# Kernel optimization log

Measured on AMD Instinct MI355X. Metric: run time of the kernel, lower is better.

The kernel has to match this reference:

```python
import jax, jax.numpy as jnp
import numpy as np

VOCAB = 40000
EMB = 128
INNER = 128
Q_LEN = 20


def setup_inputs() -> dict:
    key = jax.random.key(0)
    ks = jax.random.split(key, 16)
    B, S, NB = 32, 512, 20
    std = 0.1
    inp = {
        "memories": jax.random.normal(ks[0], (B, S, NB, EMB), jnp.float32),
        "stories": jax.random.normal(ks[1], (B, S, EMB), jnp.float32),
        "stories_mask": jnp.ones((B, S), jnp.float32),
        "queries": jax.random.randint(ks[2], (B, Q_LEN), 0, VOCAB, jnp.int32),
        "keys": jax.random.randint(ks[3], (NB,), 0, VOCAB, jnp.int32),
        # learned parameters
        "emb_table": jax.random.normal(ks[4], (VOCAB, EMB), jnp.float32) * std,
        "mult_mask": jnp.ones((Q_LEN, EMB), jnp.float32),
        "A": jax.random.normal(ks[5], (EMB, INNER), jnp.float32) * std,
        "Bm": jax.random.normal(ks[6], (EMB, INNER), jnp.float32) * std,
        "C": jax.random.normal(ks[7], (EMB, INNER), jnp.float32) * std,
        "v": jnp.ones((INNER,), jnp.float32),
        "D": jax.random.normal(ks[8], (EMB, INNER), jnp.float32) * std,
        "E": jax.random.normal(ks[9], (EMB, INNER), jnp.float32) * std,
        "F": jax.random.normal(ks[10], (EMB, INNER), jnp.float32) * std,
        "w": jnp.ones((INNER,), jnp.float32),
        "H": jax.random.normal(ks[11], (EMB, EMB), jnp.float32) * std,
        "R": jax.random.normal(ks[12], (EMB, VOCAB), jnp.float32) * std,
    }
    return inp


def reference(memories, stories, stories_mask, queries, keys,
              emb_table, mult_mask, A, Bm, C, v, D, E, F, w, H, R):
    # _reduce_query: embed tokens, apply positional multiplicative mask, sum over positions
    u = jnp.sum(emb_table[queries] * mult_mask, axis=1)            # [B, emb]

    # intratemporal (Bahdanau-style) attention over memory blocks
    ia = jnp.einsum('bsne,ei->bsni', memories, A)                  # [B,S,NB,inner]
    kb = emb_table[keys] @ Bm                                      # [NB,inner]
    qc = u @ C                                                     # [B,inner]
    intr_align = jnp.sum(v * jnp.tanh(ia + kb[None, None] + qc[:, None, None]), axis=3)  # [B,S,NB]
    intr_attn = jax.nn.softmax(intr_align, axis=2)[..., None]      # [B,S,NB,1]
    temporal_memory = jnp.sum(intr_attn * memories, axis=2)        # [B,S,emb]

    # temporal attention over story sentences (with sentence term E, softmax activation)
    td = temporal_memory @ D                                       # [B,S,inner]
    te = stories @ E                                               # [B,S,inner]
    tf = (u @ F)[:, None]                                          # [B,1,inner]
    temporal_align_unmasked = jnp.sum(w * jnp.tanh(td + te + tf), axis=2)  # [B,S]
    temporal_align = temporal_align_unmasked * stories_mask
    # softmax branch: additive -inf mask where stories_mask == 0 (inf*0 NaNs zeroed in torch)
    masked_logits = jnp.where(stories_mask != 0, temporal_align, -jnp.inf)
    temporal_attn = jax.nn.softmax(masked_logits, axis=1)          # [B,S]

    # output readout (standard memory-network head)
    o = jnp.sum(temporal_attn[..., None] * temporal_memory, axis=1)  # [B,emb]
    logits = (o + u @ H) @ R                                         # [B,vocab]
    return logits
```

## Files before the change

kernel.cpp:

```cpp
#include <hip/hip_runtime.h>
#include <hip/hip_bf16.h>

#define B_   32
#define S_   512
#define NB_  20
#define EMB_ 128
#define VOC_ 40000

typedef float f32x4 __attribute__((ext_vector_type(4)));
typedef __bf16 bf16x8 __attribute__((ext_vector_type(8)));

union Frag {
  uint4 u;
  bf16x8 b;
  unsigned short s[8];
};

__device__ __forceinline__ unsigned short f2bf(float x){
  unsigned u = __float_as_uint(x);
  unsigned r = (u + 0x7FFFu + ((u>>16)&1u)) >> 16;
  return (unsigned short)r;
}
__device__ __forceinline__ float bf2f(unsigned short s){
  return __uint_as_float(((unsigned)s)<<16);
}
__device__ __forceinline__ float tanh_fast(float x){
  float xx = fminf(fmaxf(x, -15.f), 15.f);
  float e = __expf(2.f*xx);
  return (e-1.f)/(e+1.f);
}

__global__ __launch_bounds__(128) void prep_kernel(
    const int* __restrict__ queries, const int* __restrict__ keys,
    const float* __restrict__ emb, const float* __restrict__ mmask,
    const float* __restrict__ A, const float* __restrict__ Bm,
    const float* __restrict__ C, const float* __restrict__ D,
    const float* __restrict__ E, const float* __restrict__ F,
    const float* __restrict__ H,
    float* __restrict__ qc_w, float* __restrict__ tf_w,
    float* __restrict__ uh_w, float* __restrict__ kb_w,
    unsigned short* __restrict__ afragH, unsigned short* __restrict__ afragL,
    unsigned short* __restrict__ w2fragH, unsigned short* __restrict__ w2fragL)
{
  int bid = blockIdx.x, tid = threadIdx.x;
  if (bid < 32) {
    __shared__ float ulds[128];
    int b = bid;
    float s = 0.f;
    for (int q=0;q<NB_;q++){
      int tok = queries[b*NB_+q];
      s += emb[tok*128+tid]*mmask[q*128+tid];
    }
    ulds[tid] = s;
    __syncthreads();
    float sq=0.f, sf=0.f, sh=0.f;
    for (int e=0;e<128;e++){
      float uv = ulds[e];
      sq += uv*C[e*128+tid];
      sf += uv*F[e*128+tid];
      sh += uv*H[e*128+tid];
    }
    qc_w[b*128+tid]=sq; tf_w[b*128+tid]=sf; uh_w[b*128+tid]=sh;
  } else if (bid < 52) {
    __shared__ float ek[128];
    int n = bid-32;
    int tok = keys[n];
    ek[tid] = emb[tok*128+tid];
    __syncthreads();
    float s=0.f;
    for (int e=0;e<128;e++) s += ek[e]*Bm[e*128+tid];
    kb_w[n*128+tid] = s;
  } else if (bid < 60) {
    int a = bid-52;
    for (int cc=0;cc<2;cc++){
      int c = (a*128+tid)*2+cc;
      int lane = c&63, kc = (c>>6)&3, nt = c>>8;
      int n2 = nt*16 + (lane&15);
      int k0 = kc*32 + (lane>>4)*8;
      alignas(16) unsigned short th[8], tl[8];
      #pragma unroll
      for (int j=0;j<8;j++){
        float x = A[(k0+j)*128+n2];
        unsigned short h = f2bf(x);
        th[j] = h;
        tl[j] = f2bf(x - bf2f(h));
      }
      *(uint4*)(afragH + c*8) = *(const uint4*)th;
      *(uint4*)(afragL + c*8) = *(const uint4*)tl;
    }
  } else {
    int wb = bid-60;
    for (int cc=0;cc<2;cc++){
      int c = (wb*128+tid)*2+cc;
      int lane = c&63, kc = (c>>6)&7, nt = c>>9;
      int n2 = nt*16 + (lane&15);
      int k0 = kc*32 + (lane>>4)*8;
      alignas(16) unsigned short th[8], tl[8];
      #pragma unroll
      for (int j=0;j<8;j++){
        int k = k0+j;
        float x = (k<128) ? D[k*128+n2] : E[(k-128)*128+n2];
        unsigned short h = f2bf(x);
        th[j] = h;
        tl[j] = f2bf(x - bf2f(h));
      }
      *(uint4*)(w2fragH + c*8) = *(const uint4*)th;
      *(uint4*)(w2fragL + c*8) = *(const uint4*)tl;
    }
  }
}

__global__ __launch_bounds__(256) void k2a_kernel(
    const float* __restrict__ mem,
    const unsigned short* __restrict__ afragH, const unsigned short* __restrict__ afragL,
    const float* __restrict__ kb_w, const float* __restrict__ qc_w,
    const float* __restrict__ vvec, float* __restrict__ tm_w)
{
  __shared__ unsigned short mfrH[5*4*64*8];
  __shared__ unsigned short mfrL[5*4*64*8];
  __shared__ float alignP[4*80];
  __shared__ float aligns[80];
  __shared__ float attns[80];

  int g = blockIdx.x, tid = threadIdx.x;
  int b = g >> 7;

  const float4* gm = (const float4*)(mem) + (size_t)g*2560;
  #pragma unroll
  for (int it=0; it<10; ++it){
    int i4 = tid + it*256;
    float4 d = gm[i4];
    int e4 = i4*4;
    int row = e4 >> 7;
    int k0 = e4 & 127;
    int mt = row >> 4;
    int lane = (((k0>>3)&3)<<4) | (row & 15);
    int chunk = (mt*4 + (k0>>5))*64 + lane;
    int sa = chunk*8 + (k0 & 7);
    unsigned short hx=f2bf(d.x), hy=f2bf(d.y), hz=f2bf(d.z), hw=f2bf(d.w);
    *(uint2*)(mfrH + sa) = make_uint2((unsigned)hx|((unsigned)hy<<16),
                                      (unsigned)hz|((unsigned)hw<<16));
    unsigned short lx=f2bf(d.x-bf2f(hx)), ly=f2bf(d.y-bf2f(hy));
    unsigned short lz=f2bf(d.z-bf2f(hz)), lw=f2bf(d.w-bf2f(hw));
    *(uint2*)(mfrL + sa) = make_uint2((unsigned)lx|((unsigned)ly<<16),
                                      (unsigned)lz|((unsigned)lw<<16));
  }
  __syncthreads();

  int w = tid>>6, lane = tid&63;
  int lo16_ = lane & 15, hi16_ = lane >> 4;
  int nt0 = 2*w, nt1 = 2*w+1;

  f32x4 acc[5][2];
  #pragma unroll
  for (int mt=0;mt<5;mt++){ acc[mt][0]=(f32x4)(0.f); acc[mt][1]=(f32x4)(0.f); }

  #pragma unroll
  for (int kc=0;kc<4;kc++){
    Frag b0h, b0l, b1h, b1l;
    b0h.u = *(const uint4*)(afragH + ((size_t)(nt0*4+kc)*64 + lane)*8);
    b0l.u = *(const uint4*)(afragL + ((size_t)(nt0*4+kc)*64 + lane)*8);
    b1h.u = *(const uint4*)(afragH + ((size_t)(nt1*4+kc)*64 + lane)*8);
    b1l.u = *(const uint4*)(afragL + ((size_t)(nt1*4+kc)*64 + lane)*8);
    #pragma unroll
    for (int mt=0;mt<5;mt++){
      Frag ah, al;
      ah.u = *(const uint4*)(mfrH + ((mt*4+kc)*64 + lane)*8);
      al.u = *(const uint4*)(mfrL + ((mt*4+kc)*64 + lane)*8);
      acc[mt][0] = __builtin_amdgcn_mfma_f32_16x16x32_bf16(ah.b, b0h.b, acc[mt][0], 0,0,0);
      acc[mt][0] = __builtin_amdgcn_mfma_f32_16x16x32_bf16(al.b, b0h.b, acc[mt][0], 0,0,0);
      acc[mt][0] = __builtin_amdgcn_mfma_f32_16x16x32_bf16(ah.b, b0l.b, acc[mt][0], 0,0,0);
      acc[mt][1] = __builtin_amdgcn_mfma_f32_16x16x32_bf16(ah.b, b1h.b, acc[mt][1], 0,0,0);
      acc[mt][1] = __builtin_amdgcn_mfma_f32_16x16x32_bf16(al.b, b1h.b, acc[mt][1], 0,0,0);
      acc[mt][1] = __builtin_amdgcn_mfma_f32_16x16x32_bf16(ah.b, b1l.b, acc[mt][1], 0,0,0);
    }
  }

  #pragma unroll
  for (int mt=0;mt<5;mt++){
    #pragma unroll
    for (int r=0;r<4;r++){
      unsigned row = mt*16 + hi16_*4 + r;
      unsigned p = row/20u;
      unsigned n = row - p*20u;
      float part = 0.f;
      #pragma unroll
      for (int t2=0;t2<2;t2++){
        int col = (2*w+t2)*16 + lo16_;
        float z = acc[mt][t2][r] + kb_w[n*128+col] + qc_w[b*128+col];
        part += vvec[col]*tanh_fast(z);
      }
      part += __shfl_xor(part, 1);
      part += __shfl_xor(part, 2);
      part += __shfl_xor(part, 4);
      part += __shfl_xor(part, 8);
      if (lo16_ == 0) alignP[w*80+row] = part;
    }
  }
  __syncthreads();
  if (tid < 80){
    aligns[tid] = alignP[tid] + alignP[80+tid] + alignP[160+tid] + alignP[240+tid];
  }
  __syncthreads();
  if (tid < 4){
    float mx = -1e30f;
    for (int n=0;n<NB_;n++) mx = fmaxf(mx, aligns[tid*NB_+n]);
    float s = 0.f;
    for (int n=0;n<NB_;n++){ float e = __expf(aligns[tid*NB_+n]-mx); attns[tid*NB_+n]=e; s+=e; }
    float inv = 1.f/s;
    for (int n=0;n<NB_;n++) attns[tid*NB_+n] *= inv;
  }
  __syncthreads();

  if (tid < 128){
    int p2 = tid>>5, e0 = (tid&31)*4;
    float4 o = make_float4(0.f,0.f,0.f,0.f);
    #pragma unroll
    for (int n=0;n<NB_;n++){
      int row = p2*NB_+n;
      float a = attns[row];
      int mt = row>>4;
      int lane2 = (((e0>>3)&3)<<4) | (row&15);
      int chunk = (mt*4 + (e0>>5))*64 + lane2;
      uint2 ph = *(const uint2*)(mfrH + chunk*8 + (e0&7));
      uint2 pl = *(const uint2*)(mfrL + chunk*8 + (e0&7));
      o.x += a*(bf2f((unsigned short)(ph.x&0xffffu)) + bf2f((unsigned short)(pl.x&0xffffu)));
      o.y += a*(bf2f((unsigned short)(ph.x>>16))    + bf2f((unsigned short)(pl.x>>16)));
      o.z += a*(bf2f((unsigned short)(ph.y&0xffffu)) + bf2f((unsigned short)(pl.y&0xffffu)));
      o.w += a*(bf2f((unsigned short)(ph.y>>16))    + bf2f((unsigned short)(pl.y>>16)));
    }
    *(float4*)(tm_w + ((size_t)g*4+p2)*128 + e0) = o;
  }
}

__global__ __launch_bounds__(256) void k2b_kernel(
    const float* __restrict__ tm_w, const float* __restrict__ stories,
    const unsigned short* __restrict__ w2fragH, const unsigned short* __restrict__ w2fragL,
    const float* __restrict__ tf_w, const float* __restrict__ wvec,
    const float* __restrict__ smask, float* __restrict__ talign_w)
{
  __shared__ unsigned short afrH[8*64*8];
  __shared__ unsigned short afrL[8*64*8];
  __shared__ float partial[4*16];
  int gb = blockIdx.x, tid = threadIdx.x;
  int flat0 = gb*16;
  int b = flat0 >> 9;

  #pragma unroll
  for (int cc=0;cc<2;cc++){
    int c = tid*2+cc;
    int lane = c&63, kc = c>>6;
    int p = lane&15;
    int k0 = kc*32 + (lane>>4)*8;
    const float* src = (k0 < 128)
        ? (tm_w + ((size_t)(flat0+p))*128 + k0)
        : (stories + ((size_t)(flat0+p))*128 + (k0-128));
    float4 s0 = *(const float4*)(src);
    float4 s1 = *(const float4*)(src+4);
    alignas(16) unsigned short th[8], tl[8];
    float xs[8] = {s0.x,s0.y,s0.z,s0.w,s1.x,s1.y,s1.z,s1.w};
    #pragma unroll
    for (int j=0;j<8;j++){
      unsigned short h = f2bf(xs[j]);
      th[j]=h; tl[j]=f2bf(xs[j]-bf2f(h));
    }
    *(uint4*)(afrH + c*8) = *(const uint4*)th;
    *(uint4*)(afrL + c*8) = *(const uint4*)tl;
  }
  __syncthreads();

  int w = tid>>6, lane = tid&63;
  int lo = lane&15, hi = lane>>4;
  f32x4 acc0 = (f32x4)(0.f), acc1 = (f32x4)(0.f);

  #pragma unroll
  for (int kc=0;kc<8;kc++){
    Frag ah, al, b0h, b0l, b1h, b1l;
    ah.u  = *(const uint4*)(afrH + (kc*64+lane)*8);
    al.u  = *(const uint4*)(afrL + (kc*64+lane)*8);
    b0h.u = *(const uint4*)(w2fragH + ((size_t)((2*w)*8+kc)*64+lane)*8);
    b0l.u = *(const uint4*)(w2fragL + ((size_t)((2*w)*8+kc)*64+lane)*8);
    b1h.u = *(const uint4*)(w2fragH + ((size_t)((2*w+1)*8+kc)*64+lane)*8);
    b1l.u = *(const uint4*)(w2fragL + ((size_t)((2*w+1)*8+kc)*64+lane)*8);
    acc0 = __builtin_amdgcn_mfma_f32_16x16x32_bf16(ah.b, b0h.b, acc0, 0,0,0);
    acc0 = __builtin_amdgcn_mfma_f32_16x16x32_bf16(al.b, b0h.b, acc0, 0,0,0);
    acc0 = __builtin_amdgcn_mfma_f32_16x16x32_bf16(ah.b, b0l.b, acc0, 0,0,0);
    acc1 = __builtin_amdgcn_mfma_f32_16x16x32_bf16(ah.b, b1h.b, acc1, 0,0,0);
    acc1 = __builtin_amdgcn_mfma_f32_16x16x32_bf16(al.b, b1h.b, acc1, 0,0,0);
    acc1 = __builtin_amdgcn_mfma_f32_16x16x32_bf16(ah.b, b1l.b, acc1, 0,0,0);
  }

  #pragma unroll
  for (int r=0;r<4;r++){
    int prow = hi*4+r;
    float part = 0.f;
    {
      int i0 = (2*w)*16+lo;
      part += wvec[i0]*tanh_fast(acc0[r] + tf_w[b*128+i0]);
      int i1 = (2*w+1)*16+lo;
      part += wvec[i1]*tanh_fast(acc1[r] + tf_w[b*128+i1]);
    }
    part += __shfl_xor(part,1);
    part += __shfl_xor(part,2);
    part += __shfl_xor(part,4);
    part += __shfl_xor(part,8);
    if (lo==0) partial[w*16+prow] = part;
  }
  __syncthreads();
  if (tid<16){
    float ta = partial[tid]+partial[16+tid]+partial[32+tid]+partial[48+tid];
    int flat = flat0+tid;
    float m = smask[flat];
    talign_w[flat] = (m != 0.0f) ? ta*m : -INFINITY;
  }
}

__global__ __launch_bounds__(256) void k3a_kernel(
    const float* __restrict__ talign_w, float* __restrict__ attn_w)
{
  __shared__ float red[256];
  int b = blockIdx.x, tid = threadIdx.x;
  float v0 = talign_w[b*512+tid];
  float v1 = talign_w[b*512+256+tid];
  red[tid] = fmaxf(v0,v1);
  __syncthreads();
  for (int s=128;s>0;s>>=1){ if (tid<s) red[tid]=fmaxf(red[tid],red[tid+s]); __syncthreads(); }
  float M = red[0];
  __syncthreads();
  float e0 = __expf(v0-M), e1 = __expf(v1-M);
  red[tid] = e0+e1;
  __syncthreads();
  for (int s=128;s>0;s>>=1){ if (tid<s) red[tid]+=red[tid+s]; __syncthreads(); }
  float invZ = 1.f/red[0];
  attn_w[b*512+tid] = e0*invZ;
  attn_w[b*512+256+tid] = e1*invZ;
}

__global__ __launch_bounds__(256) void k3p_kernel(
    const float* __restrict__ attn_w, const float* __restrict__ tm_w,
    float* __restrict__ opart)
{
  __shared__ float part[256];
  int bc = blockIdx.x, tid = threadIdx.x;
  int b = bc>>3, c = bc&7;
  int e = tid&127, h = tid>>7;
  float a = 0.f;
  int sbase = c*64 + h;
  #pragma unroll 4
  for (int i=0;i<32;i++){
    int s = sbase + i*2;
    a += attn_w[b*512+s]*tm_w[((size_t)(b*512+s))*128 + e];
  }
  part[tid] = a;
  __syncthreads();
  if (tid<128) opart[bc*128+tid] = part[tid]+part[tid+128];
}

__global__ __launch_bounds__(256) void k3b_kernel(
    const float* __restrict__ opart, const float* __restrict__ uh_w,
    float* __restrict__ ov_w)
{
  int idx = blockIdx.x*256 + threadIdx.x;
  int b = idx>>7, e = idx&127;
  float s = uh_w[idx];
  #pragma unroll
  for (int c=0;c<8;c++) s += opart[(b*8+c)*128 + e];
  ov_w[idx] = s;
}

__global__ __launch_bounds__(256) void k4_kernel(
    const float* __restrict__ ov_w, const float* __restrict__ R,
    float* __restrict__ out)
{
  int j = blockIdx.x*256 + threadIdx.x;
  if (j >= VOC_) return;
  float acc[32];
  #pragma unroll
  for (int b=0;b<32;b++) acc[b]=0.f;
  for (int e=0;e<128;e++){
    float r = R[(size_t)e*VOC_ + j];
    #pragma unroll
    for (int b=0;b<32;b++) acc[b] += ov_w[b*128+e]*r;
  }
  #pragma unroll
  for (int b=0;b<32;b++) out[(size_t)b*VOC_ + j] = acc[b];
}

extern "C" void kernel_launch(void* const* d_in, const int* in_sizes, int n_in,
                              void* d_out, int out_size, void* d_ws, size_t ws_size,
                              hipStream_t stream)
{
  const float* mem    = (const float*)d_in[0];
  const float* stories= (const float*)d_in[1];
  const float* smask  = (const float*)d_in[2];
  const int*   queries= (const int*)d_in[3];
  const int*   keys   = (const int*)d_in[4];
  const float* emb    = (const float*)d_in[5];
  const float* mmask  = (const float*)d_in[6];
  const float* A      = (const float*)d_in[7];
  const float* Bm     = (const float*)d_in[8];
  const float* C      = (const float*)d_in[9];
  const float* vvec   = (const float*)d_in[10];
  const float* D      = (const float*)d_in[11];
  const float* E      = (const float*)d_in[12];
  const float* F      = (const float*)d_in[13];
  const float* wvec   = (const float*)d_in[14];
  const float* H      = (const float*)d_in[15];
  const float* R      = (const float*)d_in[16];
  float* out = (float*)d_out;

  char* ws = (char*)d_ws;
  float* qc_w             = (float*)(ws + 0);
  float* tf_w             = (float*)(ws + 16384);
  float* uh_w             = (float*)(ws + 32768);
  float* kb_w             = (float*)(ws + 49152);
  unsigned short* afragH  = (unsigned short*)(ws + 60416);
  unsigned short* afragL  = (unsigned short*)(ws + 93184);
  unsigned short* w2fragH = (unsigned short*)(ws + 125952);
  unsigned short* w2fragL = (unsigned short*)(ws + 191488);
  float* tm_w             = (float*)(ws + 257024);
  float* talign_w         = (float*)(ws + 8645632);
  float* attn_w           = (float*)(ws + 8711168);
  float* opart            = (float*)(ws + 8776704);
  float* ov_w             = (float*)(ws + 8907776);

  prep_kernel<<<76,128,0,stream>>>(queries, keys, emb, mmask, A, Bm, C, D, E, F, H,
                                   qc_w, tf_w, uh_w, kb_w,
                                   afragH, afragL, w2fragH, w2fragL);
  k2a_kernel<<<4096,256,0,stream>>>(mem, afragH, afragL, kb_w, qc_w, vvec, tm_w);
  k2b_kernel<<<1024,256,0,stream>>>(tm_w, stories, w2fragH, w2fragL, tf_w, wvec, smask, talign_w);
  k3a_kernel<<<32,256,0,stream>>>(talign_w, attn_w);
  k3p_kernel<<<256,256,0,stream>>>(attn_w, tm_w, opart);
  k3b_kernel<<<16,256,0,stream>>>(opart, uh_w, ov_w);
  k4_kernel<<<157,256,0,stream>>>(ov_w, R, out);
}
```

Before: 422.9 us.

## Switch split-bf16 MFMA to single fp16, swizzle LDS, fuse k3, retile vocab GEMV

Replaces the three-pass split-bf16 (hi/lo) MFMA emulation of fp32 with a single fp16 MFMA pass in both attention kernels, which cuts matrix work and LDS traffic by roughly a factor of three. Adds an XOR swizzle to the LDS fragment layout to reduce bank conflicts. Fuses the softmax, weighted readout and residual add into one kernel. Retiles the final R projection so each block covers 64 vocab columns by 8 batch rows, giving more blocks and fewer registers per thread. Dropping to plain fp16 lowers precision, and since memories and stories are standard-normal inputs this adds error in the attention logits.

Result: faster. 376.2 us (-11.0%).

```diff
diff --git a/kernel.cpp b/kernel.cpp
--- a/kernel.cpp
+++ b/kernel.cpp
@@ -8,27 +8,26 @@
 #define VOC_ 40000
 
 typedef float f32x4 __attribute__((ext_vector_type(4)));
-typedef __bf16 bf16x8 __attribute__((ext_vector_type(8)));
-
-union Frag {
-  uint4 u;
-  bf16x8 b;
-  unsigned short s[8];
-};
-
-__device__ __forceinline__ unsigned short f2bf(float x){
-  unsigned u = __float_as_uint(x);
-  unsigned r = (u + 0x7FFFu + ((u>>16)&1u)) >> 16;
-  return (unsigned short)r;
-}
-__device__ __forceinline__ float bf2f(unsigned short s){
-  return __uint_as_float(((unsigned)s)<<16);
+typedef _Float16 f16x8 __attribute__((ext_vector_type(8)));
+typedef __fp16 fp16x2 __attribute__((ext_vector_type(2)));
+
+union FragH { uint4 u; f16x8 h; };
+union H2 { fp16x2 h; unsigned u; };
+
+__device__ __forceinline__ unsigned pk2(float a, float b){
+  H2 t; t.h = __builtin_amdgcn_cvt_pkrtz(a, b);
+  return t.u;
+}
+__device__ __forceinline__ unsigned short f2h(float x){
+  _Float16 h = (_Float16)x;
+  return __builtin_bit_cast(unsigned short, h);
 }
 __device__ __forceinline__ float tanh_fast(float x){
   float xx = fminf(fmaxf(x, -15.f), 15.f);
   float e = __expf(2.f*xx);
   return (e-1.f)/(e+1.f);
 }
+
 
 __global__ __launch_bounds__(128) void prep_kernel(
     const int* __restrict__ queries, const int* __restrict__ keys,
@@ -39,8 +38,7 @@
     const float* __restrict__ H,
     float* __restrict__ qc_w, float* __restrict__ tf_w,
     float* __restrict__ uh_w, float* __restrict__ kb_w,
-    unsigned short* __restrict__ afragH, unsigned short* __restrict__ afragL,
-    unsigned short* __restrict__ w2fragH, unsigned short* __restrict__ w2fragL)
+    unsigned short* __restrict__ afrag, unsigned short* __restrict__ w2frag)
 {
   int bid = blockIdx.x, tid = threadIdx.x;
   if (bid < 32) {
@@ -77,16 +75,10 @@
       int lane = c&63, kc = (c>>6)&3, nt = c>>8;
       int n2 = nt*16 + (lane&15);
       int k0 = kc*32 + (lane>>4)*8;
-      alignas(16) unsigned short th[8], tl[8];
+      alignas(16) unsigned short t[8];
       #pragma unroll
-      for (int j=0;j<8;j++){
-        float x = A[(k0+j)*128+n2];
-        unsigned short h = f2bf(x);
-        th[j] = h;
-        tl[j] = f2bf(x - bf2f(h));
-      }
-      *(uint4*)(afragH + c*8) = *(const uint4*)th;
-      *(uint4*)(afragL + c*8) = *(const uint4*)tl;
+      for (int j=0;j<8;j++) t[j] = f2h(A[(k0+j)*128+n2]);
+      *(uint4*)(afrag + c*8) = *(const uint4*)t;
     }
   } else {
     int wb = bid-60;
@@ -95,29 +87,24 @@
       int lane = c&63, kc = (c>>6)&7, nt = c>>9;
       int n2 = nt*16 + (lane&15);
       int k0 = kc*32 + (lane>>4)*8;
-      alignas(16) unsigned short th[8], tl[8];
+      alignas(16) unsigned short t[8];
       #pragma unroll
       for (int j=0;j<8;j++){
         int k = k0+j;
         float x = (k<128) ? D[k*128+n2] : E[(k-128)*128+n2];
-        unsigned short h = f2bf(x);
-        th[j] = h;
-        tl[j] = f2bf(x - bf2f(h));
+        t[j] = f2h(x);
       }
-      *(uint4*)(w2fragH + c*8) = *(const uint4*)th;
-      *(uint4*)(w2fragL + c*8) = *(const uint4*)tl;
+      *(uint4*)(w2frag + c*8) = *(const uint4*)t;
     }
   }
 }
 
 __global__ __launch_bounds__(256) void k2a_kernel(
-    const float* __restrict__ mem,
-    const unsigned short* __restrict__ afragH, const unsigned short* __restrict__ afragL,
+    const float* __restrict__ mem, const unsigned short* __restrict__ afrag,
     const float* __restrict__ kb_w, const float* __restrict__ qc_w,
     const float* __restrict__ vvec, float* __restrict__ tm_w)
 {
-  __shared__ unsigned short mfrH[5*4*64*8];
-  __shared__ unsigned short mfrL[5*4*64*8];
+  __shared__ unsigned short mfr[5*4*64*8];
   __shared__ float alignP[4*80];
   __shared__ float aligns[80];
   __shared__ float attns[80];
@@ -132,24 +119,17 @@
     float4 d = gm[i4];
     int e4 = i4*4;
     int row = e4 >> 7;
-    int k0 = e4 & 127;
-    int mt = row >> 4;
-    int lane = (((k0>>3)&3)<<4) | (row & 15);
-    int chunk = (mt*4 + (k0>>5))*64 + lane;
-    int sa = chunk*8 + (k0 & 7);
-    unsigned short hx=f2bf(d.x), hy=f2bf(d.y), hz=f2bf(d.z), hw=f2bf(d.w);
-    *(uint2*)(mfrH + sa) = make_uint2((unsigned)hx|((unsigned)hy<<16),
-                                      (unsigned)hz|((unsigned)hw<<16));
-    unsigned short lx=f2bf(d.x-bf2f(hx)), ly=f2bf(d.y-bf2f(hy));
-    unsigned short lz=f2bf(d.z-bf2f(hz)), lw=f2bf(d.w-bf2f(hw));
-    *(uint2*)(mfrL + sa) = make_uint2((unsigned)lx|((unsigned)ly<<16),
-                                      (unsigned)lz|((unsigned)lw<<16));
+    int k = e4 & 127;
+    int mt = row>>4, r = row&15;
+    int kg = k>>5, s2 = (k>>3)&3;
+    int slot = (s2<<4) | ((r ^ s2 ^ ((kg&1)<<2)) & 15);
+    int chunk = (mt*4+kg)*64 + slot;
+    *(uint2*)(mfr + chunk*8 + (k&7)) = make_uint2(pk2(d.x,d.y), pk2(d.z,d.w));
   }
   __syncthreads();
 
   int w = tid>>6, lane = tid&63;
-  int lo16_ = lane & 15, hi16_ = lane >> 4;
-  int nt0 = 2*w, nt1 = 2*w+1;
+  int lo16 = lane & 15, hi16 = lane >> 4;
 
   f32x4 acc[5][2];
   #pragma unroll
@@ -157,22 +137,16 @@
 
   #pragma unroll
   for (int kc=0;kc<4;kc++){
-    Frag b0h, b0l, b1h, b1l;
-    b0h.u = *(const uint4*)(afragH + ((size_t)(nt0*4+kc)*64 + lane)*8);
-    b0l.u = *(const uint4*)(afragL + ((size_t)(nt0*4+kc)*64 + lane)*8);
-    b1h.u = *(const uint4*)(afragH + ((size_t)(nt1*4+kc)*64 + lane)*8);
-    b1l.u = *(const uint4*)(afragL + ((size_t)(nt1*4+kc)*64 + lane)*8);
+    FragH b0, b1;
+    b0.u = *(const uint4*)(afrag + ((size_t)((2*w)*4+kc)*64 + lane)*8);
+    b1.u = *(const uint4*)(afrag + ((size_t)((2*w+1)*4+kc)*64 + lane)*8);
+    int slot = (hi16<<4) | ((lo16 ^ hi16 ^ ((kc&1)<<2)) & 15);
     #pragma unroll
     for (int mt=0;mt<5;mt++){
-      Frag ah, al;
-      ah.u = *(const uint4*)(mfrH + ((mt*4+kc)*64 + lane)*8);
-      al.u = *(const uint4*)(mfrL + ((mt*4+kc)*64 + lane)*8);
-      acc[mt][0] = __builtin_amdgcn_mfma_f32_16x16x32_bf16(ah.b, b0h.b, acc[mt][0], 0,0,0);
-      acc[mt][0] = __builtin_amdgcn_mfma_f32_16x16x32_bf16(al.b, b0h.b, acc[mt][0], 0,0,0);
-      acc[mt][0] = __builtin_amdgcn_mfma_f32_16x16x32_bf16(ah.b, b0l.b, acc[mt][0], 0,0,0);
-      acc[mt][1] = __builtin_amdgcn_mfma_f32_16x16x32_bf16(ah.b, b1h.b, acc[mt][1], 0,0,0);
-      acc[mt][1] = __builtin_amdgcn_mfma_f32_16x16x32_bf16(al.b, b1h.b, acc[mt][1], 0,0,0);
-      acc[mt][1] = __builtin_amdgcn_mfma_f32_16x16x32_bf16(ah.b, b1l.b, acc[mt][1], 0,0,0);
+      FragH a;
+      a.u = *(const uint4*)(mfr + ((mt*4+kc)*64 + slot)*8);
+      acc[mt][0] = __builtin_amdgcn_mfma_f32_16x16x32_f16(a.h, b0.h, acc[mt][0], 0,0,0);
+      acc[mt][1] = __builtin_amdgcn_mfma_f32_16x16x32_f16(a.h, b1.h, acc[mt][1], 0,0,0);
     }
   }
 
@@ -180,13 +154,13 @@
   for (int mt=0;mt<5;mt++){
     #pragma unroll
     for (int r=0;r<4;r++){
-      unsigned row = mt*16 + hi16_*4 + r;
+      unsigned row = mt*16 + hi16*4 + r;
       unsigned p = row/20u;
       unsigned n = row - p*20u;
       float part = 0.f;
       #pragma unroll
       for (int t2=0;t2<2;t2++){
-        int col = (2*w+t2)*16 + lo16_;
+        int col = (2*w+t2)*16 + lo16;
         float z = acc[mt][t2][r] + kb_w[n*128+col] + qc_w[b*128+col];
         part += vvec[col]*tanh_fast(z);
       }
@@ -194,7 +168,7 @@
       part += __shfl_xor(part, 2);
       part += __shfl_xor(part, 4);
       part += __shfl_xor(part, 8);
-      if (lo16_ == 0) alignP[w*80+row] = part;
+      if (lo16 == 0) alignP[w*80+row] = part;
     }
   }
   __syncthreads();
@@ -214,20 +188,21 @@
 
   if (tid < 128){
     int p2 = tid>>5, e0 = (tid&31)*4;
+    int kg = e0>>5, s2 = (e0>>3)&3;
     float4 o = make_float4(0.f,0.f,0.f,0.f);
     #pragma unroll
     for (int n=0;n<NB_;n++){
       int row = p2*NB_+n;
       float a = attns[row];
-      int mt = row>>4;
-      int lane2 = (((e0>>3)&3)<<4) | (row&15);
-      int chunk = (mt*4 + (e0>>5))*64 + lane2;
-      uint2 ph = *(const uint2*)(mfrH + chunk*8 + (e0&7));
-      uint2 pl = *(const uint2*)(mfrL + chunk*8 + (e0&7));
-      o.x += a*(bf2f((unsigned short)(ph.x&0xffffu)) + bf2f((unsigned short)(pl.x&0xffffu)));
-      o.y += a*(bf2f((unsigned short)(ph.x>>16))    + bf2f((unsigned short)(pl.x>>16)));
-      o.z += a*(bf2f((unsigned short)(ph.y&0xffffu)) + bf2f((unsigned short)(pl.y&0xffffu)));
-      o.w += a*(bf2f((unsigned short)(ph.y>>16))    + bf2f((unsigned short)(pl.y>>16)));
+      int mt = row>>4, r = row&15;
+      int slot = (s2<<4) | ((r ^ s2 ^ ((kg&1)<<2)) & 15);
+      int chunk = (mt*4+kg)*64 + slot;
+      uint2 pk = *(const uint2*)(mfr + chunk*8 + (e0&7));
+      H2 q0, q1; q0.u = pk.x; q1.u = pk.y;
+      o.x += a*(float)q0.h[0];
+      o.y += a*(float)q0.h[1];
+      o.z += a*(float)q1.h[0];
+      o.w += a*(float)q1.h[1];
     }
     *(float4*)(tm_w + ((size_t)g*4+p2)*128 + e0) = o;
   }
@@ -235,20 +210,19 @@
 
 __global__ __launch_bounds__(256) void k2b_kernel(
     const float* __restrict__ tm_w, const float* __restrict__ stories,
-    const unsigned short* __restrict__ w2fragH, const unsigned short* __restrict__ w2fragL,
-    const float* __restrict__ tf_w, const float* __restrict__ wvec,
-    const float* __restrict__ smask, float* __restrict__ talign_w)
-{
-  __shared__ unsigned short afrH[8*64*8];
-  __shared__ unsigned short afrL[8*64*8];
+    const unsigned short* __restrict__ w2frag, const float* __restrict__ tf_w,
+    const float* __restrict__ wvec, const float* __restrict__ smask,
+    float* __restrict__ talign_w)
+{
+  __shared__ unsigned short afr[512*8];
   __shared__ float partial[4*16];
   int gb = blockIdx.x, tid = threadIdx.x;
   int flat0 = gb*16;
   int b = flat0 >> 9;
 
   #pragma unroll
-  for (int cc=0;cc<2;cc++){
-    int c = tid*2+cc;
+  for (int it=0;it<2;it++){
+    int c = tid + it*256;
     int lane = c&63, kc = c>>6;
     int p = lane&15;
     int k0 = kc*32 + (lane>>4)*8;
@@ -257,15 +231,10 @@
         : (stories + ((size_t)(flat0+p))*128 + (k0-128));
     float4 s0 = *(const float4*)(src);
     float4 s1 = *(const float4*)(src+4);
-    alignas(16) unsigned short th[8], tl[8];
-    float xs[8] = {s0.x,s0.y,s0.z,s0.w,s1.x,s1.y,s1.z,s1.w};
-    #pragma unroll
-    for (int j=0;j<8;j++){
-      unsigned short h = f2bf(xs[j]);
-      th[j]=h; tl[j]=f2bf(xs[j]-bf2f(h));
-    }
-    *(uint4*)(afrH + c*8) = *(const uint4*)th;
-    *(uint4*)(afrL + c*8) = *(const uint4*)tl;
+    uint4 pkd;
+    pkd.x = pk2(s0.x,s0.y); pkd.y = pk2(s0.z,s0.w);
+    pkd.z = pk2(s1.x,s1.y); pkd.w = pk2(s1.z,s1.w);
+    *(uint4*)(afr + c*8) = pkd;
   }
   __syncthreads();
 
@@ -275,19 +244,12 @@
 
   #pragma unroll
   for (int kc=0;kc<8;kc++){
-    Frag ah, al, b0h, b0l, b1h, b1l;
-    ah.u  = *(const uint4*)(afrH + (kc*64+lane)*8);
-    al.u  = *(const uint4*)(afrL + (kc*64+lane)*8);
-    b0h.u = *(const uint4*)(w2fragH + ((size_t)((2*w)*8+kc)*64+lane)*8);
-    b0l.u = *(const uint4*)(w2fragL + ((size_t)((2*w)*8+kc)*64+lane)*8);
-    b1h.u = *(const uint4*)(w2fragH + ((size_t)((2*w+1)*8+kc)*64+lane)*8);
-    b1l.u = *(const uint4*)(w2fragL + ((size_t)((2*w+1)*8+kc)*64+lane)*8);
-    acc0 = __builtin_amdgcn_mfma_f32_16x16x32_bf16(ah.b, b0h.b, acc0, 0,0,0);
-    acc0 = __builtin_amdgcn_mfma_f32_16x16x32_bf16(al.b, b0h.b, acc0, 0,0,0);
-    acc0 = __builtin_amdgcn_mfma_f32_16x16x32_bf16(ah.b, b0l.b, acc0, 0,0,0);
-    acc1 = __builtin_amdgcn_mfma_f32_16x16x32_bf16(ah.b, b1h.b, acc1, 0,0,0);
-    acc1 = __builtin_amdgcn_mfma_f32_16x16x32_bf16(al.b, b1h.b, acc1, 0,0,0);
-    acc1 = __builtin_amdgcn_mfma_f32_16x16x32_bf16(ah.b, b1l.b, acc1, 0,0,0);
+    FragH af, b0, b1;
+    af.u = *(const uint4*)(afr + (kc*64+lane)*8);
+    b0.u = *(const uint4*)(w2frag + ((size_t)((2*w)*8+kc)*64+lane)*8);
+    b1.u = *(const uint4*)(w2frag + ((size_t)((2*w+1)*8+kc)*64+lane)*8);
+    acc0 = __builtin_amdgcn_mfma_f32_16x16x32_f16(af.h, b0.h, acc0, 0,0,0);
+    acc1 = __builtin_amdgcn_mfma_f32_16x16x32_f16(af.h, b1.h, acc1, 0,0,0);
   }
 
   #pragma unroll
@@ -315,9 +277,11 @@
   }
 }
 
-__global__ __launch_bounds__(256) void k3a_kernel(
-    const float* __restrict__ talign_w, float* __restrict__ attn_w)
-{
+__global__ __launch_bounds__(256) void k3_kernel(
+    const float* __restrict__ talign_w, const float* __restrict__ tm_w,
+    const float* __restrict__ uh_w, float* __restrict__ ov_w)
+{
+  __shared__ float attn[512];
   __shared__ float red[256];
   int b = blockIdx.x, tid = threadIdx.x;
   float v0 = talign_w[b*512+tid];
@@ -332,58 +296,46 @@
   __syncthreads();
   for (int s=128;s>0;s>>=1){ if (tid<s) red[tid]+=red[tid+s]; __syncthreads(); }
   float invZ = 1.f/red[0];
-  attn_w[b*512+tid] = e0*invZ;
-  attn_w[b*512+256+tid] = e1*invZ;
-}
-
-__global__ __launch_bounds__(256) void k3p_kernel(
-    const float* __restrict__ attn_w, const float* __restrict__ tm_w,
-    float* __restrict__ opart)
-{
-  __shared__ float part[256];
-  int bc = blockIdx.x, tid = threadIdx.x;
-  int b = bc>>3, c = bc&7;
+  attn[tid] = e0*invZ;
+  attn[256+tid] = e1*invZ;
+  __syncthreads();
+
   int e = tid&127, h = tid>>7;
+  const float* tmb = tm_w + ((size_t)b*512 + h*256)*128 + e;
   float a = 0.f;
-  int sbase = c*64 + h;
   #pragma unroll 4
-  for (int i=0;i<32;i++){
-    int s = sbase + i*2;
-    a += attn_w[b*512+s]*tm_w[((size_t)(b*512+s))*128 + e];
-  }
-  part[tid] = a;
-  __syncthreads();
-  if (tid<128) opart[bc*128+tid] = part[tid]+part[tid+128];
-}
-
-__global__ __launch_bounds__(256) void k3b_kernel(
-    const float* __restrict__ opart, const float* __restrict__ uh_w,
-    float* __restrict__ ov_w)
-{
-  int idx = blockIdx.x*256 + threadIdx.x;
-  int b = idx>>7, e = idx&127;
-  float s = uh_w[idx];
-  #pragma unroll
-  for (int c=0;c<8;c++) s += opart[(b*8+c)*128 + e];
-  ov_w[idx] = s;
+  for (int i=0;i<256;i++){
+    a += attn[h*256+i]*tmb[(size_t)i*128];
+  }
+  red[tid] = a;
+  __syncthreads();
+  if (tid<128) ov_w[b*128+tid] = red[tid]+red[128+tid]+uh_w[b*128+tid];
 }
 
 __global__ __launch_bounds__(256) void k4_kernel(
     const float* __restrict__ ov_w, const float* __restrict__ R,
     float* __restrict__ out)
 {
-  int j = blockIdx.x*256 + threadIdx.x;
-  if (j >= VOC_) return;
-  float acc[32];
-  #pragma unroll
-  for (int b=0;b<32;b++) acc[b]=0.f;
-  for (int e=0;e<128;e++){
-    float r = R[(size_t)e*VOC_ + j];
+  int tid = threadIdx.x;
+  int j = blockIdx.x*64 + (tid&63);
+  int bh = tid>>6;
+  const float* ovb = ov_w + bh*8*128;
+  float acc[8];
+  #pragma unroll
+  for (int bb=0;bb<8;bb++) acc[bb]=0.f;
+  for (int e=0;e<128;e+=4){
+    float r0 = R[(size_t)(e+0)*VOC_ + j];
+    float r1 = R[(size_t)(e+1)*VOC_ + j];
+    float r2 = R[(size_t)(e+2)*VOC_ + j];
+    float r3 = R[(size_t)(e+3)*VOC_ + j];
     #pragma unroll
-    for (int b=0;b<32;b++) acc[b] += ov_w[b*128+e]*r;
-  }
-  #pragma unroll
-  for (int b=0;b<32;b++) out[(size_t)b*VOC_ + j] = acc[b];
+    for (int bb=0;bb<8;bb++){
+      acc[bb] += ovb[bb*128+e+0]*r0 + ovb[bb*128+e+1]*r1
+               + ovb[bb*128+e+2]*r2 + ovb[bb*128+e+3]*r3;
+    }
+  }
+  #pragma unroll
+  for (int bb=0;bb<8;bb++) out[(size_t)(bh*8+bb)*VOC_ + j] = acc[bb];
 }
 
 extern "C" void kernel_launch(void* const* d_in, const int* in_sizes, int n_in,
@@ -414,23 +366,16 @@
   float* tf_w             = (float*)(ws + 16384);
   float* uh_w             = (float*)(ws + 32768);
   float* kb_w             = (float*)(ws + 49152);
-  unsigned short* afragH  = (unsigned short*)(ws + 60416);
-  unsigned short* afragL  = (unsigned short*)(ws + 93184);
-  unsigned short* w2fragH = (unsigned short*)(ws + 125952);
-  unsigned short* w2fragL = (unsigned short*)(ws + 191488);
-  float* tm_w             = (float*)(ws + 257024);
-  float* talign_w         = (float*)(ws + 8645632);
-  float* attn_w           = (float*)(ws + 8711168);
-  float* opart            = (float*)(ws + 8776704);
-  float* ov_w             = (float*)(ws + 8907776);
+  unsigned short* afrag   = (unsigned short*)(ws + 60416);
+  unsigned short* w2frag  = (unsigned short*)(ws + 93184);
+  float* tm_w             = (float*)(ws + 158720);
+  float* talign_w         = (float*)(ws + 8547328);
+  float* ov_w             = (float*)(ws + 8612864);
 
   prep_kernel<<<76,128,0,stream>>>(queries, keys, emb, mmask, A, Bm, C, D, E, F, H,
-                                   qc_w, tf_w, uh_w, kb_w,
-                                   afragH, afragL, w2fragH, w2fragL);
-  k2a_kernel<<<4096,256,0,stream>>>(mem, afragH, afragL, kb_w, qc_w, vvec, tm_w);
-  k2b_kernel<<<1024,256,0,stream>>>(tm_w, stories, w2fragH, w2fragL, tf_w, wvec, smask, talign_w);
-  k3a_kernel<<<32,256,0,stream>>>(talign_w, attn_w);
-  k3p_kernel<<<256,256,0,stream>>>(attn_w, tm_w, opart);
-  k3b_kernel<<<16,256,0,stream>>>(opart, uh_w, ov_w);
-  k4_kernel<<<157,256,0,stream>>>(ov_w, R, out);
-}
+                                   qc_w, tf_w, uh_w, kb_w, afrag, w2frag);
+  k2a_kernel<<<4096,256,0,stream>>>(mem, afrag, kb_w, qc_w, vvec, tm_w);
+  k2b_kernel<<<1024,256,0,stream>>>(tm_w, stories, w2frag, tf_w, wvec, smask, talign_w);
+  k3_kernel<<<32,256,0,stream>>>(talign_w, tm_w, uh_w, ov_w);
+  k4_kernel<<<625,256,0,stream>>>(ov_w, R, out);
+}
```
